# Kernel optimization log

Measured on AMD Instinct MI355X. Metric: run time of the kernel, lower is better.

Reference implementation:

```python
import jax, jax.numpy as jnp
import numpy as np

B, N, D, H, L = 8, 1025, 1024, 8, 2   # N = maxlen + 1
NUM_BUCKETS = 64
EPS = 1e-8


def layernorm(x):
    mu = jnp.mean(x, axis=-1, keepdims=True)
    var = jnp.mean((x - mu) ** 2, axis=-1, keepdims=True)
    return (x - mu) / jnp.sqrt(var + EPS)


def rmsnorm(x):
    return x * jax.lax.rsqrt(jnp.mean(x * x, axis=-1, keepdims=True) + EPS)


def rel_attn_bias(action_ts, ts_w, pos_w):
    # positional part: pos_w[j - i + N - 1]  (equivalent to the pad/repeat trick)
    idx = jnp.arange(N)[None, :] - jnp.arange(N)[:, None] + (N - 1)  # [N,N] in [0,2N-2]
    rel_pos = pos_w[idx][None]  # [1,N,N]
    # time part: bucketize ext[i+1] - ext[j], ext = cat(ts, ts[:, N-1:N])
    ext = jnp.concatenate([action_ts, action_ts[:, N - 1:N]], axis=1)  # [B,N+1]
    diff = ext[:, 1:, None] - ext[:, None, :-1]  # [B,N,N]
    bucket = (jnp.log(jnp.clip(jnp.abs(diff), 1, None).astype(jnp.float32)) / 0.301).astype(jnp.int32)
    bucket = jnp.clip(bucket, 0, NUM_BUCKETS)
    rel_ts = ts_w[bucket]  # [B,N,N]
    return rel_pos + rel_ts


def hstu_block(x, mask, bias, qkvu, out_w, out_b, fc1_w, fc1_b, fc2_w, fc2_b):
    hd = D // H
    xn = layernorm(x)
    qkvu_act = jax.nn.silu(xn @ qkvu)  # [B,N,4D]
    q, k, v, u = jnp.split(qkvu_act, 4, axis=-1)
    q = q.reshape(B, N, H, hd)
    k = k.reshape(B, N, H, hd)
    v = v.reshape(B, N, H, hd)
    scores = jnp.einsum('bihd,bjhd->bhij', q, k) + bias[:, None]  # [B,H,N,N]
    attn = jax.nn.silu(scores) / N * mask[:, None]
    av = jnp.einsum('bhij,bjhd->bihd', attn, v).reshape(B, N, D)
    attn_out = (u * layernorm(av)) @ out_w + out_b
    h = x + attn_out
    # SwiGLU FFN (mult=2) with RMSNorm pre-norm and residual
    vg = rmsnorm(h) @ fc1_w + fc1_b  # [B,N,4D]
    vv, g = jnp.split(vg, 2, axis=-1)
    y = (jax.nn.silu(g) * vv) @ fc2_w + fc2_b
    return h + y


def setup_inputs() -> dict:
    key = jax.random.key(0)
    ks = jax.random.split(key, 12)
    std = 0.02
    seqs = jax.random.normal(ks[0], (B, N, D), jnp.float32)
    mask = jnp.tril(jnp.ones((N, N), jnp.float32))[None].repeat(B, axis=0)
    action_ts = jnp.sort(jax.random.randint(ks[1], (B, N), 0, 1000000000).astype(jnp.int64), axis=1)
    return {
        'seqs': seqs,
        'mask': mask,
        'action_ts': action_ts,
        'qkvu': jax.random.normal(ks[2], (L, D, 4 * D), jnp.float32) * std,
        'out_w': jax.random.normal(ks[3], (L, D, D), jnp.float32) * std,
        'out_b': jnp.zeros((L, D), jnp.float32),
        'ts_w': jax.random.normal(ks[4], (L, NUM_BUCKETS + 1), jnp.float32) * std,
        'pos_w': jax.random.normal(ks[5], (L, 2 * N - 1), jnp.float32) * std,
        'fc1_w': jax.random.normal(ks[6], (L, D, 4 * D), jnp.float32) * std,
        'fc1_b': jnp.zeros((L, 4 * D), jnp.float32),
        'fc2_w': jax.random.normal(ks[7], (L, 2 * D, D), jnp.float32) * std,
        'fc2_b': jnp.zeros((L, D), jnp.float32),
    }


def reference(seqs, mask, action_ts, qkvu, out_w, out_b, ts_w, pos_w, fc1_w, fc1_b, fc2_w, fc2_b):
    h = seqs
    for l in range(L):
        bias = rel_attn_bias(action_ts, ts_w[l], pos_w[l])
        h = hstu_block(h, mask, bias, qkvu[l], out_w[l], out_b[l],
                       fc1_w[l], fc1_b[l], fc2_w[l], fc2_b[l])
    return h
```

## Files before the change

### kernel.cpp

```cpp
#include <hip/hip_runtime.h>
#include <hip/hip_bf16.h>
#include <math.h>

#define BB 8
#define SEQN 1025
#define DD 1024
#define HH 8
#define HD 128
#define LL 2
#define MROWS (BB*SEQN)
#define NBUCKET 64

using short8 = __attribute__((ext_vector_type(8))) short;
using f32x4  = __attribute__((ext_vector_type(4))) float;
using f32x16 = __attribute__((ext_vector_type(16))) float;

__device__ __forceinline__ float silu_f(float x) { return x / (1.f + expf(-x)); }

__device__ __forceinline__ float bf2f(ushort u) {
  union { uint i; float f; } x; x.i = ((uint)u) << 16; return x.f;
}
__device__ __forceinline__ ushort f2bf(float f) {
  __hip_bfloat16 b = __float2bfloat16(f);
  return *reinterpret_cast<ushort*>(&b);
}
__device__ __forceinline__ void gll16(const void* g, void* l) {
  __builtin_amdgcn_global_load_lds((const __attribute__((address_space(1))) void*)g,
                                   (__attribute__((address_space(3))) void*)l, 16, 0, 0);
}
__device__ __forceinline__ uint pkbf(float lo, float hi) {
  uint r;
  asm("v_cvt_pk_bf16_f32 %0, %1, %2" : "=v"(r) : "v"(lo), "v"(hi));
  return r;
}
__device__ __forceinline__ f32x16 z16() {
  f32x16 v;
#pragma unroll
  for (int i = 0; i < 16; ++i) v[i] = 0.f;
  return v;
}

__global__ __launch_bounds__(256) void copy_kernel(const float* __restrict__ in,
                                                   float* __restrict__ out, int n4) {
  int idx = blockIdx.x * blockDim.x + threadIdx.x;
  int stride = gridDim.x * blockDim.x;
  const float4* i4 = (const float4*)in;
  float4* o4 = (float4*)out;
  for (int i = idx; i < n4; i += stride) o4[i] = i4[i];
}

__global__ __launch_bounds__(256) void wtrans(const float* __restrict__ W,
                                              ushort* __restrict__ Wt, int K, int N) {
  __shared__ float tile[32][33];
  int tid = threadIdx.x;
  int tx = tid & 31, ty = tid >> 5;
  int n0 = blockIdx.x * 32, k0 = blockIdx.y * 32;
#pragma unroll
  for (int r = 0; r < 32; r += 8)
    tile[ty + r][tx] = W[(size_t)(k0 + ty + r) * N + n0 + tx];
  __syncthreads();
#pragma unroll
  for (int r = 0; r < 32; r += 8)
    Wt[(size_t)(n0 + ty + r) * K + k0 + tx] = f2bf(tile[tx][ty + r]);
}

__global__ __launch_bounds__(256) void bias_kernel(const int* __restrict__ ts,
    const float* __restrict__ ts_w, const float* __restrict__ pos_w,
    float* __restrict__ biasT)
{
  int i = blockIdx.x * 256 + threadIdx.x;
  int j = blockIdx.y;
  int b = blockIdx.z;
  if (i >= SEQN) return;
  int ip1 = i + 1; if (ip1 > SEQN - 1) ip1 = SEQN - 1;
  long long t1 = (long long)ts[b * SEQN + ip1];
  long long t0 = (long long)ts[b * SEQN + j];
  long long d = t1 - t0;
  if (d < 0) d = -d;
  if (d < 1) d = 1;
  int bucket = (int)(logf((float)d) / 0.301f);
  if (bucket < 0) bucket = 0;
  if (bucket > NBUCKET) bucket = NBUCKET;
  biasT[((size_t)(b * SEQN + j)) * SEQN + i] = pos_w[j - i + SEQN - 1] + ts_w[bucket];
}

__global__ __launch_bounds__(256) void ln_kernel(const float* __restrict__ in,
                                                 ushort* __restrict__ out) {
  int row = blockIdx.x;
  int tid = threadIdx.x;
  const float* x = in + (size_t)row * DD;
  float4 v = *(const float4*)&x[tid * 4];
  float s = v.x + v.y + v.z + v.w;
  float ss = v.x*v.x + v.y*v.y + v.z*v.z + v.w*v.w;
#pragma unroll
  for (int off = 32; off >= 1; off >>= 1) { s += __shfl_xor(s, off); ss += __shfl_xor(ss, off); }
  __shared__ float red0[4], red1[4];
  if ((tid & 63) == 0) { red0[tid >> 6] = s; red1[tid >> 6] = ss; }
  __syncthreads();
  s = red0[0] + red0[1] + red0[2] + red0[3];
  ss = red1[0] + red1[1] + red1[2] + red1[3];
  float mu = s * (1.f / DD);
  float var = fmaxf(ss * (1.f / DD) - mu * mu, 0.f);
  float inv = 1.f / sqrtf(var + 1e-8f);
  ushort4 o;
  o.x = f2bf((v.x - mu) * inv); o.y = f2bf((v.y - mu) * inv);
  o.z = f2bf((v.z - mu) * inv); o.w = f2bf((v.w - mu) * inv);
  *(ushort4*)&out[(size_t)row * DD + tid * 4] = o;
}

__global__ __launch_bounds__(256) void rms_kernel(const float* __restrict__ in,
                                                  ushort* __restrict__ out) {
  int row = blockIdx.x;
  int tid = threadIdx.x;
  const float* x = in + (size_t)row * DD;
  float4 v = *(const float4*)&x[tid * 4];
  float ss = v.x*v.x + v.y*v.y + v.z*v.z + v.w*v.w;
#pragma unroll
  for (int off = 32; off >= 1; off >>= 1) ss += __shfl_xor(ss, off);
  __shared__ float red1[4];
  if ((tid & 63) == 0) red1[tid >> 6] = ss;
  __syncthreads();
  ss = red1[0] + red1[1] + red1[2] + red1[3];
  float inv = 1.f / sqrtf(ss * (1.f / DD) + 1e-8f);
  ushort4 o;
  o.x = f2bf(v.x * inv); o.y = f2bf(v.y * inv);
  o.z = f2bf(v.z * inv); o.w = f2bf(v.w * inv);
  *(ushort4*)&out[(size_t)row * DD + tid * 4] = o;
}

__global__ __launch_bounds__(256) void uln_kernel(const float* __restrict__ av,
    const ushort* __restrict__ act, ushort* __restrict__ out) {
  int row = blockIdx.x;
  int tid = threadIdx.x;
  const float* x = av + (size_t)row * DD;
  float4 v = *(const float4*)&x[tid * 4];
  float s = v.x + v.y + v.z + v.w;
  float ss = v.x*v.x + v.y*v.y + v.z*v.z + v.w*v.w;
#pragma unroll
  for (int off = 32; off >= 1; off >>= 1) { s += __shfl_xor(s, off); ss += __shfl_xor(ss, off); }
  __shared__ float red0[4], red1[4];
  if ((tid & 63) == 0) { red0[tid >> 6] = s; red1[tid >> 6] = ss; }
  __syncthreads();
  s = red0[0] + red0[1] + red0[2] + red0[3];
  ss = red1[0] + red1[1] + red1[2] + red1[3];
  float mu = s * (1.f / DD);
  float var = fmaxf(ss * (1.f / DD) - mu * mu, 0.f);
  float inv = 1.f / sqrtf(var + 1e-8f);
  ushort4 uu = *(const ushort4*)&act[(size_t)row * 4096 + 3072 + tid * 4];
  ushort4 o;
  o.x = f2bf(bf2f(uu.x) * (v.x - mu) * inv);
  o.y = f2bf(bf2f(uu.y) * (v.y - mu) * inv);
  o.z = f2bf(bf2f(uu.z) * (v.z - mu) * inv);
  o.w = f2bf(bf2f(uu.w) * (v.w - mu) * inv);
  *(ushort4*)&out[(size_t)row * DD + tid * 4] = o;
}

__global__ __launch_bounds__(256) void gated_kernel(const ushort* __restrict__ act,
                                                    ushort* __restrict__ gated) {
  int idx = blockIdx.x * 256 + threadIdx.x;
  const int total = MROWS * 2048 / 8;
  if (idx >= total) return;
  int row = idx >> 8;
  int col = (idx & 255) * 8;
  const ushort* base = act + (size_t)row * 4096;
  short8 vv = *(const short8*)(base + col);
  short8 gg = *(const short8*)(base + 2048 + col);
  short8 o;
#pragma unroll
  for (int j = 0; j < 8; ++j) {
    float v = bf2f((ushort)vv[j]);
    float g = bf2f((ushort)gg[j]);
    o[j] = (short)f2bf(silu_f(g) * v);
  }
  *(short8*)&gated[(size_t)row * 2048 + col] = o;
}

template<int MODE, int BM, int BN>
__global__ __launch_bounds__(512, 2) void mgemm2(const ushort* __restrict__ A,
    const ushort* __restrict__ Bt, const float* __restrict__ bvec,
    void* __restrict__ Cout, int M, int Nn, int K)
{
  constexpr int ACH = BM / 64;
  constexpr int BCH = BN / 64;
  constexpr int MF  = BM / 32;
  constexpr int NF  = BN / 64;
  constexpr int AUS = BM * 64;
  constexpr int LDSU = (BM + BN) * 64;
  __shared__ ushort LS[2][LDSU];

  const int tid = threadIdx.x;
  const int lane = tid & 63, wave = tid >> 6;
  const int wm = wave >> 2, wn = wave & 3;
  const int lrow = lane & 15, lk = lane >> 4;
  const int bm = blockIdx.y * BM, bn = blockIdx.x * BN;

  const ushort* Ag[ACH]; const ushort* Bg[BCH];
  int Ald[ACH], Bld[BCH];
#pragma unroll
  for (int i = 0; i < ACH; ++i) {
    int c = tid + 512 * i, row = c >> 3, s = c & 7;
    Ag[i] = A + (size_t)(bm + row) * K + (s ^ (row & 7)) * 8;
    Ald[i] = c * 8;
  }
#pragma unroll
  for (int i = 0; i < BCH; ++i) {
    int c = tid + 512 * i, row = c >> 3, s = c & 7;
    Bg[i] = Bt + (size_t)(bn + row) * K + (s ^ (row & 7)) * 8;
    Bld[i] = AUS + c * 8;
  }
  int aoff[MF], boff[NF];
#pragma unroll
  for (int m = 0; m < MF; ++m) {
    int row = wm * (BM / 2) + m * 16 + lrow;
    aoff[m] = row * 64 + ((lk ^ (lrow & 7)) * 8);
  }
#pragma unroll
  for (int n = 0; n < NF; ++n) {
    int row = wn * (BN / 4) + n * 16 + lrow;
    boff[n] = AUS + row * 64 + ((lk ^ (lrow & 7)) * 8);
  }

  f32x4 acc[MF][NF];
#pragma unroll
  for (int m = 0; m < MF; ++m)
#pragma unroll
    for (int n = 0; n < NF; ++n) acc[m][n] = (f32x4){0.f, 0.f, 0.f, 0.f};

  const int NT = K >> 6;

#define STAGE_TILE(T, B)                                        \
  {                                                             \
    const int _ko = (T) << 6;                                   \
    _Pragma("unroll")                                           \
    for (int i = 0; i < ACH; ++i) gll16(Ag[i] + _ko, &LS[B][Ald[i]]); \
    _Pragma("unroll")                                           \
    for (int i = 0; i < BCH; ++i) gll16(Bg[i] + _ko, &LS[B][Bld[i]]); \
  }

  STAGE_TILE(0, 0);
  __syncthreads();
  for (int t = 0; t < NT; ++t) {
    const int buf = t & 1;
    if (t + 1 < NT) STAGE_TILE(t + 1, buf ^ 1);
    short8 bfr[NF][2];
#pragma unroll
    for (int n = 0; n < NF; ++n) {
      bfr[n][0] = *(const short8*)&LS[buf][boff[n]];
      bfr[n][1] = *(const short8*)&LS[buf][boff[n] ^ 32];
    }
#pragma unroll
    for (int m = 0; m < MF; ++m) {
      short8 af0 = *(const short8*)&LS[buf][aoff[m]];
      short8 af1 = *(const short8*)&LS[buf][aoff[m] ^ 32];
      __builtin_amdgcn_s_setprio(1);
#pragma unroll
      for (int n = 0; n < NF; ++n) {
        acc[m][n] = __builtin_amdgcn_mfma_f32_16x16x32_bf16(af0, bfr[n][0], acc[m][n], 0, 0, 0);
        acc[m][n] = __builtin_amdgcn_mfma_f32_16x16x32_bf16(af1, bfr[n][1], acc[m][n], 0, 0, 0);
      }
      __builtin_amdgcn_s_setprio(0);
    }
    __syncthreads();
  }
#undef STAGE_TILE

  const int rowb0 = bm + wm * (BM / 2) + lk * 4;
  const int colb0 = bn + wn * (BN / 4) + lrow;
  if (MODE == 1) {
    float* Cf = (float*)Cout;
#pragma unroll
    for (int m = 0; m < MF; ++m) {
      int row0 = rowb0 + m * 16;
#pragma unroll
      for (int n = 0; n < NF; ++n) {
        int col = colb0 + n * 16;
        float bv = bvec[col];
#pragma unroll
        for (int r = 0; r < 4; ++r) {
          int row = row0 + r;
          if (row < M) {
            float* p = Cf + (size_t)row * Nn + col;
            *p += acc[m][n][r] + bv;
          }
        }
      }
    }
  } else {
    __hip_bfloat16* Cb = (__hip_bfloat16*)Cout;
#pragma unroll
    for (int m = 0; m < MF; ++m) {
      int row0 = rowb0 + m * 16;
#pragma unroll
      for (int n = 0; n < NF; ++n) {
        int col = colb0 + n * 16;
        float bv = (MODE == 2) ? bvec[col] : 0.f;
#pragma unroll
        for (int r = 0; r < 4; ++r) {
          int row = row0 + r;
          if (row < M) {
            float v = acc[m][n][r];
            float o = (MODE == 0) ? silu_f(v) : (v + bv);
            Cb[(size_t)row * Nn + col] = __float2bfloat16(o);
          }
        }
      }
    }
  }
}

__global__ __launch_bounds__(256) void attn_kernel(const ushort* __restrict__ act,
    const float* __restrict__ biasT, float* __restrict__ av)
{
  __shared__ __align__(16) char KL[8192];
  __shared__ __align__(16) char VL[8320];
  const int tid = threadIdx.x;
  const int l = tid & 63, w = tid >> 6;
  const int qi = (int)(gridDim.x - 1 - blockIdx.x);
  const int i0 = qi * 128;
  const int h = blockIdx.y, b = blockIdx.z;
  const int lo31 = l & 31, hi = l >> 5;

  const int jlim = (i0 + 128 < SEQN) ? i0 + 128 : SEQN;
  const int nt = (jlim + 31) >> 5;

  const int gi_q = i0 + w * 32 + lo31;
  const int gi_qc = gi_q < SEQN ? gi_q : SEQN - 1;
  const size_t actB = (size_t)b * SEQN;
  const ushort* qrow = act + (actB + gi_qc) * 4096 + h * HD;
  short8 qreg[8];
#pragma unroll
  for (int dc = 0; dc < 8; ++dc)
    qreg[dc] = *(const short8*)(qrow + dc * 16 + hi * 8);

  f32x16 acc[4];
#pragma unroll
  for (int dt = 0; dt < 4; ++dt) acc[dt] = z16();

  const int id0 = tid, id1 = tid + 256;
  const int j_0 = id0 >> 4, c8_0 = (id0 & 15) * 8;
  const int j_1 = id1 >> 4, c8_1 = (id1 & 15) * 8;
  char* kw0 = KL + j_0 * 256 + (((id0 & 15) ^ (j_0 & 15)) << 4);
  char* kw1 = KL + j_1 * 256 + (((id1 & 15) ^ (j_1 & 15)) << 4);
  char* vw0 = VL + ((id0 & 15) >> 1) * 1040 + j_0 * 32 + (id0 & 1) * 16;
  char* vw1 = VL + ((id1 & 15) >> 1) * 1040 + j_1 * 32 + (id1 & 1) * 16;
  const uint vbase = (uint)(size_t)(__attribute__((address_space(3))) char*)
      (VL + ((l >> 4) & 1) * 1040 + hi * 256 + (l & 15) * 8);

  short8 kr0, kr1, vr0, vr1;
  {
    const ushort* p0 = act + (actB + j_0) * 4096 + 1024 + h * HD + c8_0;
    const ushort* p1 = act + (actB + j_1) * 4096 + 1024 + h * HD + c8_1;
    kr0 = *(const short8*)p0; vr0 = *(const short8*)(p0 + 1024);
    kr1 = *(const short8*)p1; vr1 = *(const short8*)(p1 + 1024);
  }
  const float invN = 1.f / (float)SEQN;
  const int gi0w = i0 + w * 32;

  for (int t = 0; t < nt; ++t) {
    const int j0 = t * 32;
    __syncthreads();
    *(short8*)kw0 = kr0; *(short8*)kw1 = kr1;
    *(short8*)vw0 = vr0; *(short8*)vw1 = vr1;
    __syncthreads();
    if (t + 1 < nt) {
      const ushort* p0 = act + (actB + j0 + 32 + j_0) * 4096 + 1024 + h * HD + c8_0;
      const ushort* p1 = act + (actB + j0 + 32 + j_1) * 4096 + 1024 + h * HD + c8_1;
      kr0 = *(const short8*)p0; vr0 = *(const short8*)(p0 + 1024);
      kr1 = *(const short8*)p1; vr1 = *(const short8*)(p1 + 1024);
    }
    if (j0 <= gi0w + 31 && gi0w < SEQN) {
      float bv[16];
#pragma unroll
      for (int r = 0; r < 16; ++r) {
        int j = (r & 3) + 8 * (r >> 2) + 4 * hi;
        int gj = j0 + j;
        int gjc = gj < SEQN ? gj : SEQN - 1;
        bv[r] = biasT[(actB + gjc) * SEQN + gi_qc];
      }
      f32x16 st = z16();
#pragma unroll
      for (int dc = 0; dc < 8; ++dc) {
        short8 kf = *(const short8*)(KL + lo31 * 256 + ((((dc << 1) + hi) ^ (lo31 & 15)) << 4));
        st = __builtin_amdgcn_mfma_f32_32x32x16_bf16(kf, qreg[dc], st, 0, 0, 0);
      }
      float p[16];
#pragma unroll
      for (int r = 0; r < 16; ++r) {
        int j = (r & 3) + 8 * (r >> 2) + 4 * hi;
        int gj = j0 + j;
        float s = st[r] + bv[r];
        float pw = s * __builtin_amdgcn_rcpf(1.f + __expf(-s)) * invN;
        p[r] = ((gj <= gi_q) && (gi_q < SEQN)) ? pw : 0.f;
      }
      short8 paf[2];
#pragma unroll
      for (int g = 0; g < 2; ++g) {
        uint w0 = pkbf(p[g * 8 + 0], p[g * 8 + 1]);
        uint w2 = pkbf(p[g * 8 + 4], p[g * 8 + 5]);
        uint w1 = pkbf(p[g * 8 + 2], p[g * 8 + 3]);
        uint w3 = pkbf(p[g * 8 + 6], p[g * 8 + 7]);
        asm volatile("v_permlane32_swap_b32 %0, %1" : "+v"(w0), "+v"(w2));
        asm volatile("v_permlane32_swap_b32 %0, %1" : "+v"(w1), "+v"(w3));
        union UF { uint u[4]; short8 s; } uf;
        uf.u[0] = w0; uf.u[1] = w1; uf.u[2] = w2; uf.u[3] = w3;
        paf[g] = uf.s;
      }
      uint64_t v00, v01, v02, v03, v10, v11, v12, v13, v20, v21, v22, v23, v30, v31, v32, v33;
      asm volatile(
        "ds_read_b64_tr_b16 %0, %16 offset:0\n\t"
        "ds_read_b64_tr_b16 %1, %16 offset:128\n\t"
        "ds_read_b64_tr_b16 %2, %16 offset:512\n\t"
        "ds_read_b64_tr_b16 %3, %16 offset:640\n\t"
        "ds_read_b64_tr_b16 %4, %16 offset:2080\n\t"
        "ds_read_b64_tr_b16 %5, %16 offset:2208\n\t"
        "ds_read_b64_tr_b16 %6, %16 offset:2592\n\t"
        "ds_read_b64_tr_b16 %7, %16 offset:2720\n\t"
        "ds_read_b64_tr_b16 %8, %16 offset:4160\n\t"
        "ds_read_b64_tr_b16 %9, %16 offset:4288\n\t"
        "ds_read_b64_tr_b16 %10, %16 offset:4672\n\t"
        "ds_read_b64_tr_b16 %11, %16 offset:4800\n\t"
        "ds_read_b64_tr_b16 %12, %16 offset:6240\n\t"
        "ds_read_b64_tr_b16 %13, %16 offset:6368\n\t"
        "ds_read_b64_tr_b16 %14, %16 offset:6752\n\t"
        "ds_read_b64_tr_b16 %15, %16 offset:6880\n\t"
        "s_waitcnt lgkmcnt(0)"
        : "=v"(v00), "=v"(v01), "=v"(v02), "=v"(v03),
          "=v"(v10), "=v"(v11), "=v"(v12), "=v"(v13),
          "=v"(v20), "=v"(v21), "=v"(v22), "=v"(v23),
          "=v"(v30), "=v"(v31), "=v"(v32), "=v"(v33)
        : "v"(vbase) : "memory");
      union UV { uint64_t q[2]; short8 s; };
      { UV uv; uv.q[0] = v00; uv.q[1] = v01;
        acc[0] = __builtin_amdgcn_mfma_f32_32x32x16_bf16(paf[0], uv.s, acc[0], 0, 0, 0); }
      { UV uv; uv.q[0] = v02; uv.q[1] = v03;
        acc[0] = __builtin_amdgcn_mfma_f32_32x32x16_bf16(paf[1], uv.s, acc[0], 0, 0, 0); }
      { UV uv; uv.q[0] = v10; uv.q[1] = v11;
        acc[1] = __builtin_amdgcn_mfma_f32_32x32x16_bf16(paf[0], uv.s, acc[1], 0, 0, 0); }
      { UV uv; uv.q[0] = v12; uv.q[1] = v13;
        acc[1] = __builtin_amdgcn_mfma_f32_32x32x16_bf16(paf[1], uv.s, acc[1], 0, 0, 0); }
      { UV uv; uv.q[0] = v20; uv.q[1] = v21;
        acc[2] = __builtin_amdgcn_mfma_f32_32x32x16_bf16(paf[0], uv.s, acc[2], 0, 0, 0); }
      { UV uv; uv.q[0] = v22; uv.q[1] = v23;
        acc[2] = __builtin_amdgcn_mfma_f32_32x32x16_bf16(paf[1], uv.s, acc[2], 0, 0, 0); }
      { UV uv; uv.q[0] = v30; uv.q[1] = v31;
        acc[3] = __builtin_amdgcn_mfma_f32_32x32x16_bf16(paf[0], uv.s, acc[3], 0, 0, 0); }
      { UV uv; uv.q[0] = v32; uv.q[1] = v33;
        acc[3] = __builtin_amdgcn_mfma_f32_32x32x16_bf16(paf[1], uv.s, acc[3], 0, 0, 0); }
    }
  }
#pragma unroll
  for (int dt = 0; dt < 4; ++dt) {
#pragma unroll
    for (int r = 0; r < 16; ++r) {
      int q = (r & 3) + 8 * (r >> 2) + 4 * hi;
      int gi = i0 + w * 32 + q;
      if (gi < SEQN)
        av[(actB + gi) * DD + h * HD + dt * 32 + lo31] = acc[dt][r];
    }
  }
}

extern "C" void kernel_launch(void* const* d_in, const int* in_sizes, int n_in,
                              void* d_out, int out_size, void* d_ws, size_t ws_size,
                              hipStream_t stream) {
  const float* seqs  = (const float*)d_in[0];
  const int*   ts    = (const int*)d_in[2];
  const float* qkvuW = (const float*)d_in[3];
  const float* outW  = (const float*)d_in[4];
  const float* outB  = (const float*)d_in[5];
  const float* tsW   = (const float*)d_in[6];
  const float* posW  = (const float*)d_in[7];
  const float* fc1W  = (const float*)d_in[8];
  const float* fc1B  = (const float*)d_in[9];
  const float* fc2W  = (const float*)d_in[10];
  const float* fc2B  = (const float*)d_in[11];
  float* h = (float*)d_out;
  char* ws = (char*)d_ws;

  ushort* xn    = (ushort*)(ws);
  ushort* act   = (ushort*)(ws + 17301504);
  ushort* gated = (ushort*)(ws + 84475904);
  float*  biasT = (float*) (ws + 118554624);
  float*  av    = (float*) (ws + 152174624);
  ushort* wq    = (ushort*)(ws + 185761824);
  ushort* wo    = (ushort*)(ws + 194150432);
  ushort* wf1   = (ushort*)(ws + 196247584);
  ushort* wf2   = (ushort*)(ws + 204636192);

  copy_kernel<<<2048, 256, 0, stream>>>(seqs, h, MROWS * DD / 4);

  for (int l = 0; l < LL; l++) {
    wtrans<<<dim3(128, 32), 256, 0, stream>>>(qkvuW + (size_t)l * DD * 4096, wq, DD, 4096);
    wtrans<<<dim3(32, 32),  256, 0, stream>>>(outW  + (size_t)l * DD * DD,   wo, DD, DD);
    wtrans<<<dim3(128, 32), 256, 0, stream>>>(fc1W  + (size_t)l * DD * 4096, wf1, DD, 4096);
    wtrans<<<dim3(32, 64),  256, 0, stream>>>(fc2W  + (size_t)l * 2048 * DD, wf2, 2048, DD);

    bias_kernel<<<dim3(5, SEQN, BB), 256, 0, stream>>>(
        ts, tsW + l * (NBUCKET + 1), posW + l * (2 * SEQN - 1), biasT);

    ln_kernel<<<MROWS, 256, 0, stream>>>(h, xn);
    mgemm2<0, 256, 256><<<dim3(16, 33), 512, 0, stream>>>(xn, wq, nullptr, act, MROWS, 4096, DD);
    attn_kernel<<<dim3(9, HH, BB), 256, 0, stream>>>(act, biasT, av);
    uln_kernel<<<MROWS, 256, 0, stream>>>(av, act, xn);
    mgemm2<1, 128, 256><<<dim3(4, 65), 512, 0, stream>>>(xn, wo, outB + l * DD, h, MROWS, DD, DD);
    rms_kernel<<<MROWS, 256, 0, stream>>>(h, xn);
    mgemm2<2, 256, 256><<<dim3(16, 33), 512, 0, stream>>>(xn, wf1, fc1B + (size_t)l * 4096, act, MROWS, 4096, DD);
    gated_kernel<<<8200, 256, 0, stream>>>(act, gated);
    mgemm2<1, 128, 256><<<dim3(4, 65), 512, 0, stream>>>(gated, wf2, fc2B + l * DD, h, MROWS, DD, 2048);
  }
}
```

Before: 1.146 ms.

## Fuse SwiGLU gating into fc1 GEMM epilogue and add 128x128 GEMM for N=1024

The fc1 GEMM now loads interleaved value/gate weight rows, so each block computes matching v and g columns and writes silu(g)*v straight to the gated buffer. This removes the separate gated kernel and the round trip of the 4096-wide fc1 activation through memory. The out-proj and fc2 GEMMs move to a new 128x128-tile, 256-thread kernel with a 3-stage async load pipeline, giving twice as many blocks for the N=1024 shape. The interleaved weight indexing and the epilogue mapping have to line up exactly for results to stay correct.

```diff
diff --git a/kernel.cpp b/kernel.cpp
--- a/kernel.cpp
+++ b/kernel.cpp
@@ -155,24 +155,111 @@
   *(ushort4*)&out[(size_t)row * DD + tid * 4] = o;
 }
 
-__global__ __launch_bounds__(256) void gated_kernel(const ushort* __restrict__ act,
-                                                    ushort* __restrict__ gated) {
-  int idx = blockIdx.x * 256 + threadIdx.x;
-  const int total = MROWS * 2048 / 8;
-  if (idx >= total) return;
-  int row = idx >> 8;
-  int col = (idx & 255) * 8;
-  const ushort* base = act + (size_t)row * 4096;
-  short8 vv = *(const short8*)(base + col);
-  short8 gg = *(const short8*)(base + 2048 + col);
-  short8 o;
-#pragma unroll
-  for (int j = 0; j < 8; ++j) {
-    float v = bf2f((ushort)vv[j]);
-    float g = bf2f((ushort)gg[j]);
-    o[j] = (short)f2bf(silu_f(g) * v);
-  }
-  *(short8*)&gated[(size_t)row * 2048 + col] = o;
+__global__ __launch_bounds__(256) void mgemm1(const ushort* __restrict__ A,
+    const ushort* __restrict__ Bt, const float* __restrict__ bvec,
+    float* __restrict__ Cout, int M, int Nn, int K)
+{
+  __shared__ ushort As[3][4096];
+  __shared__ ushort Bs[3][4096];
+  const int tid  = threadIdx.x;
+  const int lane = tid & 63, wave = tid >> 6;
+  const int wm = wave >> 1, wn = wave & 1;
+  const int lrow = lane & 15, lk = lane >> 4;
+  const int bm = blockIdx.y * 128, bn = blockIdx.x * 128;
+
+  const ushort* Aga[2]; const ushort* Bga[2];
+  ushort* Ada[2]; ushort* Bda[2];
+#pragma unroll
+  for (int i = 0; i < 2; ++i) {
+    int c = tid + 256 * i;
+    int row = c >> 2, s = c & 3;
+    int sc = s ^ ((row >> 1) & 3);
+    Aga[i] = A  + (size_t)(bm + row) * K + sc * 8;
+    Bga[i] = Bt + (size_t)(bn + row) * K + sc * 8;
+    Ada[i] = &As[0][c * 8];
+    Bda[i] = &Bs[0][c * 8];
+  }
+
+  int aoff[4], boff[4];
+#pragma unroll
+  for (int m = 0; m < 4; ++m)
+    aoff[m] = (wm * 64 + m * 16 + lrow) * 32 + ((lk ^ ((lrow >> 1) & 3)) * 8);
+#pragma unroll
+  for (int n = 0; n < 4; ++n)
+    boff[n] = (wn * 64 + n * 16 + lrow) * 32 + ((lk ^ ((lrow >> 1) & 3)) * 8);
+
+  f32x4 acc[4][4];
+#pragma unroll
+  for (int m = 0; m < 4; ++m)
+#pragma unroll
+    for (int n = 0; n < 4; ++n) acc[m][n] = (f32x4){0.f, 0.f, 0.f, 0.f};
+
+  const int nk = K >> 5;
+#pragma unroll
+  for (int t = 0; t < 2; ++t) {
+#pragma unroll
+    for (int i = 0; i < 2; ++i) {
+      gll16(Aga[i] + (t << 5), Ada[i] + t * 4096);
+      gll16(Bga[i] + (t << 5), Bda[i] + t * 4096);
+    }
+  }
+  int cur = 0, nxt2 = 2;
+  for (int kt = 0; kt < nk; ++kt) {
+    if (kt + 1 < nk) {
+      asm volatile("s_waitcnt vmcnt(4)" ::: "memory");
+    } else {
+      asm volatile("s_waitcnt vmcnt(0)" ::: "memory");
+    }
+    __builtin_amdgcn_s_barrier();
+    __builtin_amdgcn_sched_barrier(0);
+    if (kt + 2 < nk) {
+      const int ko = (kt + 2) << 5;
+      const int bo = nxt2 * 4096;
+#pragma unroll
+      for (int i = 0; i < 2; ++i) {
+        gll16(Aga[i] + ko, Ada[i] + bo);
+        gll16(Bga[i] + ko, Bda[i] + bo);
+      }
+    }
+    __builtin_amdgcn_s_setprio(1);
+    {
+      short8 af[4], bfr[4];
+      const int co = cur * 4096;
+#pragma unroll
+      for (int m = 0; m < 4; ++m) af[m]  = *(const short8*)&As[0][co + aoff[m]];
+#pragma unroll
+      for (int n = 0; n < 4; ++n) bfr[n] = *(const short8*)&Bs[0][co + boff[n]];
+#pragma unroll
+      for (int m = 0; m < 4; ++m)
+#pragma unroll
+        for (int n = 0; n < 4; ++n)
+          acc[m][n] = __builtin_amdgcn_mfma_f32_16x16x32_bf16(af[m], bfr[n], acc[m][n], 0, 0, 0);
+    }
+    __builtin_amdgcn_s_setprio(0);
+    __builtin_amdgcn_sched_barrier(0);
+    cur = (cur == 2) ? 0 : cur + 1;
+    nxt2 = (nxt2 == 2) ? 0 : nxt2 + 1;
+  }
+
+  const int colbase = bn + wn * 64 + lrow;
+  const int rowbase = bm + wm * 64 + lk * 4;
+#pragma unroll
+  for (int m = 0; m < 4; ++m) {
+    int row0 = rowbase + m * 16;
+#pragma unroll
+    for (int n = 0; n < 4; ++n) {
+      int col = colbase + n * 16;
+      float bv = bvec[col];
+#pragma unroll
+      for (int r = 0; r < 4; ++r) {
+        int row = row0 + r;
+        if (row < M) {
+          float* p = Cout + (size_t)row * Nn + col;
+          *p += acc[m][n][r] + bv;
+        }
+      }
+    }
+  }
 }
 
 template<int MODE, int BM, int BN>
@@ -205,7 +292,13 @@
 #pragma unroll
   for (int i = 0; i < BCH; ++i) {
     int c = tid + 512 * i, row = c >> 3, s = c & 7;
-    Bg[i] = Bt + (size_t)(bn + row) * K + (s ^ (row & 7)) * 8;
+    int gr;
+    if (MODE == 3) {
+      gr = blockIdx.x * 128 + (row >> 5) * 16 + ((row >> 4) & 1) * 2048 + (row & 15);
+    } else {
+      gr = bn + row;
+    }
+    Bg[i] = Bt + (size_t)gr * K + (s ^ (row & 7)) * 8;
     Bld[i] = AUS + c * 8;
   }
   int aoff[MF], boff[NF];
@@ -265,42 +358,40 @@
 #undef STAGE_TILE
 
   const int rowb0 = bm + wm * (BM / 2) + lk * 4;
-  const int colb0 = bn + wn * (BN / 4) + lrow;
-  if (MODE == 1) {
-    float* Cf = (float*)Cout;
+  if (MODE == 0) {
+    const int colb0 = bn + wn * (BN / 4) + lrow;
+    __hip_bfloat16* Cb = (__hip_bfloat16*)Cout;
 #pragma unroll
     for (int m = 0; m < MF; ++m) {
       int row0 = rowb0 + m * 16;
 #pragma unroll
       for (int n = 0; n < NF; ++n) {
         int col = colb0 + n * 16;
-        float bv = bvec[col];
+#pragma unroll
+        for (int r = 0; r < 4; ++r) {
+          int row = row0 + r;
+          if (row < M)
+            Cb[(size_t)row * Nn + col] = __float2bfloat16(silu_f(acc[m][n][r]));
+        }
+      }
+    }
+  } else {
+    __hip_bfloat16* Cb = (__hip_bfloat16*)Cout;
+#pragma unroll
+    for (int q = 0; q < 2; ++q) {
+      int vcol = blockIdx.x * 128 + (2 * wn + q) * 16 + lrow;
+      float bvv = bvec[vcol];
+      float bvg = bvec[vcol + 2048];
+#pragma unroll
+      for (int m = 0; m < MF; ++m) {
+        int row0 = rowb0 + m * 16;
 #pragma unroll
         for (int r = 0; r < 4; ++r) {
           int row = row0 + r;
           if (row < M) {
-            float* p = Cf + (size_t)row * Nn + col;
-            *p += acc[m][n][r] + bv;
-          }
-        }
-      }
-    }
-  } else {
-    __hip_bfloat16* Cb = (__hip_bfloat16*)Cout;
-#pragma unroll
-    for (int m = 0; m < MF; ++m) {
-      int row0 = rowb0 + m * 16;
-#pragma unroll
-      for (int n = 0; n < NF; ++n) {
-        int col = colb0 + n * 16;
-        float bv = (MODE == 2) ? bvec[col] : 0.f;
-#pragma unroll
-        for (int r = 0; r < 4; ++r) {
-          int row = row0 + r;
-          if (row < M) {
-            float v = acc[m][n][r];
-            float o = (MODE == 0) ? silu_f(v) : (v + bv);
-            Cb[(size_t)row * Nn + col] = __float2bfloat16(o);
+            float v = acc[m][2 * q][r] + bvv;
+            float g = acc[m][2 * q + 1][r] + bvg;
+            Cb[(size_t)row * 2048 + vcol] = __float2bfloat16(silu_f(g) * v);
           }
         }
       }
@@ -502,10 +593,9 @@
     mgemm2<0, 256, 256><<<dim3(16, 33), 512, 0, stream>>>(xn, wq, nullptr, act, MROWS, 4096, DD);
     attn_kernel<<<dim3(9, HH, BB), 256, 0, stream>>>(act, biasT, av);
     uln_kernel<<<MROWS, 256, 0, stream>>>(av, act, xn);
-    mgemm2<1, 128, 256><<<dim3(4, 65), 512, 0, stream>>>(xn, wo, outB + l * DD, h, MROWS, DD, DD);
+    mgemm1<<<dim3(8, 65), 256, 0, stream>>>(xn, wo, outB + l * DD, h, MROWS, DD, DD);
     rms_kernel<<<MROWS, 256, 0, stream>>>(h, xn);
-    mgemm2<2, 256, 256><<<dim3(16, 33), 512, 0, stream>>>(xn, wf1, fc1B + (size_t)l * 4096, act, MROWS, 4096, DD);
-    gated_kernel<<<8200, 256, 0, stream>>>(act, gated);
-    mgemm2<1, 128, 256><<<dim3(4, 65), 512, 0, stream>>>(gated, wf2, fc2B + l * DD, h, MROWS, DD, 2048);
-  }
-}
+    mgemm2<3, 256, 256><<<dim3(16, 33), 512, 0, stream>>>(xn, wf1, fc1B + (size_t)l * 4096, gated, MROWS, 2048, DD);
+    mgemm1<<<dim3(8, 65), 256, 0, stream>>>(gated, wf2, fc2B + l * DD, h, MROWS, DD, 2048);
+  }
+}
```

New measurement: 1.083 ms. -5.5%, faster.
